# Performance work log

Hardware: AMD Instinct MI355X
Metric: run time of the kernel (lower is better)

## Reference

```python
import jax, jax.numpy as jnp
import numpy as np

B, DT, DV, DA = 32768, 768, 512, 384
P, HID, HEADS = 128, 256, 4
HD = P // HEADS
EPS = 1e-5


def _proj_block(x, W, b, lnw, lnb):
    # Linear -> LayerNorm -> ReLU (Dropout is identity in eval)
    h = x @ W.T + b
    mu = jnp.mean(h, axis=-1, keepdims=True)
    var = jnp.var(h, axis=-1, keepdims=True)
    h = lnw * (h - mu) * jax.lax.rsqrt(var + EPS) + lnb
    return jax.nn.relu(h)


def _mha1(q, kv, Wqkv, bqkv, Wo, bo):
    # torch.nn.MultiheadAttention with seq_len=1 for both query and key/value.
    Wq, Wk, Wv = jnp.split(Wqkv, 3, axis=0)
    bq, bk, bv = jnp.split(bqkv, 3, axis=0)
    qp = (q @ Wq.T + bq).reshape(-1, HEADS, HD)   # [B,H,hd]
    kp = (kv @ Wk.T + bk).reshape(-1, HEADS, HD)
    vp = (kv @ Wv.T + bv).reshape(-1, HEADS, HD)
    scores = jnp.einsum('bhd,bhd->bh', qp, kp) * np.float32(1.0 / np.sqrt(HD))
    attn = jax.nn.softmax(scores[..., None], axis=-1)  # single key -> ones
    ctx = (attn * vp).reshape(-1, P)
    return ctx @ Wo.T + bo


def _forward(xt, xv, xa,
             Wt, bt, lnw_t, lnb_t,
             Wv_, bv_, lnw_v, lnb_v,
             Wa, ba, lnw_a, lnb_a,
             W_qkv, b_qkv, W_o, b_o,
             Wg, bg, Wf1, bf1, Wf2, bf2, Wout, bout):
    t = _proj_block(xt, Wt, bt, lnw_t, lnb_t)   # [B,P]
    v = _proj_block(xv, Wv_, bv_, lnw_v, lnb_v)
    a = _proj_block(xa, Wa, ba, lnw_a, lnb_a)
    # branch order: tv, ta, vt, va, at, av
    Qs = jnp.stack([t, t, v, v, a, a])          # [6,B,P]
    KVs = jnp.stack([v, a, t, a, t, v])
    ctx = jax.vmap(_mha1)(Qs, KVs, W_qkv, b_qkv, W_o, b_o)  # [6,B,P]
    ctx_b = jnp.transpose(ctx, (1, 0, 2))       # [B,6,P]
    feats = ctx_b.reshape(-1, 6 * P)
    g = jax.nn.softmax(feats @ Wg.T + bg, axis=-1)          # [B,6]
    gated = (ctx_b * g[:, :, None]).reshape(-1, 6 * P)
    h = jax.nn.relu(gated @ Wf1.T + bf1)
    h = jax.nn.relu(h @ Wf2.T + bf2)
    return h @ Wout.T + bout                    # [B,2]


def setup_inputs() -> dict:
    key = jax.random.key(0)
    ks = jax.random.split(key, 16)
    f32 = jnp.float32
    def n(k, shape, s=0.02):
        return jax.random.normal(k, shape, f32) * s
    return {
        'xt': jax.random.normal(ks[0], (B, DT), f32),
        'xv': jax.random.normal(ks[1], (B, DV), f32),
        'xa': jax.random.normal(ks[2], (B, DA), f32),
        'Wt': n(ks[3], (P, DT)), 'bt': jnp.zeros(P, f32),
        'lnw_t': jnp.ones(P, f32), 'lnb_t': jnp.zeros(P, f32),
        'Wv_': n(ks[4], (P, DV)), 'bv_': jnp.zeros(P, f32),
        'lnw_v': jnp.ones(P, f32), 'lnb_v': jnp.zeros(P, f32),
        'Wa': n(ks[5], (P, DA)), 'ba': jnp.zeros(P, f32),
        'lnw_a': jnp.ones(P, f32), 'lnb_a': jnp.zeros(P, f32),
        'W_qkv': n(ks[6], (6, 3 * P, P)), 'b_qkv': jnp.zeros((6, 3 * P), f32),
        'W_o': n(ks[7], (6, P, P)), 'b_o': jnp.zeros((6, P), f32),
        'Wg': n(ks[8], (6, 6 * P)), 'bg': jnp.zeros(6, f32),
        'Wf1': n(ks[9], (HID, 6 * P)), 'bf1': jnp.zeros(HID, f32),
        'Wf2': n(ks[10], (HID, HID)), 'bf2': jnp.zeros(HID, f32),
        'Wout': n(ks[11], (2, HID)), 'bout': jnp.zeros(2, f32),
    }


def reference(xt, xv, xa, Wt, bt, lnw_t, lnb_t, Wv_, bv_, lnw_v, lnb_v,
              Wa, ba, lnw_a, lnb_a, W_qkv, b_qkv, W_o, b_o,
              Wg, bg, Wf1, bf1, Wf2, bf2, Wout, bout):
    return _forward(xt, xv, xa, Wt, bt, lnw_t, lnb_t, Wv_, bv_, lnw_v, lnb_v,
                    Wa, ba, lnw_a, lnb_a, W_qkv, b_qkv, W_o, b_o,
                    Wg, bg, Wf1, bf1, Wf2, bf2, Wout, bout)
```

## Files before the change

### kernel.cpp

```cpp
#include <hip/hip_runtime.h>
#include <math.h>

#define DI __device__ __forceinline__

namespace {

constexpr int PB = 32768;

typedef _Float16 half_t;
typedef float f32x4 __attribute__((ext_vector_type(4)));
typedef _Float16 f16x8 __attribute__((ext_vector_type(8)));

#define MFMA16 __builtin_amdgcn_mfma_f32_16x16x32_f16

DI void gl16(const void* g, void* l) {
  __builtin_amdgcn_global_load_lds((const __attribute__((address_space(1))) void*)g,
                                   (__attribute__((address_space(3))) void*)l, 16, 0, 0);
}
DI f16x8 asH(f32x4 v) { return __builtin_bit_cast(f16x8, v); }

DI size_t fragIdx1(int c, int k, int P) {
  return (size_t)((k >> 5)*(P >> 4) + (c >> 4))*512
       + ((k >> 3) & 3)*128 + (c & 15)*8 + (k & 7);
}


__global__ void k_weff(const float* __restrict__ Wqkv, const float* __restrict__ bqkv,
                       const float* __restrict__ Wo, const float* __restrict__ bo,
                       float* __restrict__ M, float* __restrict__ beff)
{
  const int i = blockIdx.x >> 7;
  const int c = blockIdx.x & 127;
  const int k = threadIdx.x;
  const float* wo_row = Wo + (size_t)(i*128 + c)*128;
  const float* wv = Wqkv + (size_t)(i*384 + 256)*128;
  float acc = 0.f;
#pragma unroll 4
  for (int j = 0; j < 128; ++j)
    acc = fmaf(wo_row[j], wv[j*128 + k], acc);
  M[(size_t)(i*128 + c)*128 + k] = acc;

  __shared__ float red[128];
  const float* bv = bqkv + i*384 + 256;
  red[k] = wo_row[k] * bv[k];
  __syncthreads();
  for (int s = 64; s > 0; s >>= 1) {
    if (k < s) red[k] += red[k + s];
    __syncthreads();
  }
  if (k == 0) beff[i*128 + c] = red[0] + bo[i*128 + c];
}

__global__ void k_nbig2(const float* __restrict__ Wf1, const float* __restrict__ M,
                        const float* __restrict__ beff, half_t* __restrict__ Nf)
{
  const int i = blockIdx.x >> 8;
  const int c = blockIdx.x & 255;
  const int k = threadIdx.x;
  const float* w_row = Wf1 + (size_t)c*768 + i*128;
  const float* Mi = M + (size_t)i*128*128;
  float acc = 0.f;
#pragma unroll 4
  for (int j = 0; j < 128; ++j)
    acc = fmaf(w_row[j], Mi[j*128 + k], acc);
  Nf[fragIdx1(c, i*128 + k, 256)] = (half_t)(acc * 4096.f);

  __shared__ float red[128];
  red[k] = w_row[k] * beff[i*128 + k];
  __syncthreads();
  for (int s = 64; s > 0; s >>= 1) {
    if (k < s) red[k] += red[k + s];
    __syncthreads();
  }
  if (k == 0)
    Nf[fragIdx1(c, 768 + i, 256)] = (half_t)(red[0] * 4096.f);
  if (i == 0 && k < 26)
    Nf[fragIdx1(c, 774 + k, 256)] = (half_t)0.f;
}

__global__ void k_ghat(const float* __restrict__ M, const float* __restrict__ Wg,
                       float* __restrict__ Ghat)
{
  const int j = blockIdx.x / 3;
  const int src = blockIdx.x % 3;
  const int k = threadIdx.x;
  int i0, i1;
  if (src == 0)      { i0 = 2; i1 = 4; }
  else if (src == 1) { i0 = 0; i1 = 5; }
  else               { i0 = 1; i1 = 3; }
  float acc = 0.f;
  for (int t = 0; t < 2; ++t) {
    const int i = t ? i1 : i0;
    const float* Mi = M + (size_t)i*128*128;
    const float* wg = Wg + j*768 + i*128;
#pragma unroll 4
    for (int c = 0; c < 128; ++c)
      acc = fmaf(Mi[c*128 + k], wg[c], acc);
  }
  Ghat[j*384 + src*128 + k] = acc;
}

__global__ void k_svec(const float* __restrict__ beff, const float* __restrict__ Wg,
                       const float* __restrict__ bg, float* __restrict__ svec)
{
  const int j = blockIdx.x;
  const int c = threadIdx.x;
  float p = 0.f;
#pragma unroll
  for (int i = 0; i < 6; ++i)
    p = fmaf(beff[i*128 + c], Wg[j*768 + i*128 + c], p);
  __shared__ float red[128];
  red[c] = p;
  __syncthreads();
  for (int s = 64; s > 0; s >>= 1) {
    if (c < s) red[c] += red[c + s];
    __syncthreads();
  }
  if (c == 0) svec[j] = red[0] + bg[j];
}

__global__ void k_splitf(const float* __restrict__ in, half_t* __restrict__ outb,
                         float scale, int P, int KD)
{
  const int idx = blockIdx.x*256 + threadIdx.x;
  if (idx >= P*KD) return;
  const int c = idx / KD, k = idx - c*KD;
  outb[fragIdx1(c, k, P)] = (half_t)(in[idx] * scale);
}

template<int KD>
DI void proj_body(const float* __restrict__ X, const half_t* __restrict__ BF,
                  const float* __restrict__ bias,
                  const float* __restrict__ lnw, const float* __restrict__ lnb,
                  const float* __restrict__ Ghat, float* __restrict__ tva,
                  float* __restrict__ zpart, int row0, int colOff, int srcIdx,
                  f32x4* Bs)
{
  const int tid = threadIdx.x;
  const int lane = tid & 63, wid = tid >> 6;
  const int l15 = lane & 15, l4 = lane >> 4;
  constexpr int NT = KD >> 5;
  constexpr int NP = NT >> 2;
  const int r0 = row0 + wid*32;

  const float* xr0 = X + (size_t)(r0 + l15)*KD + l4*8;
  const float* xr1 = X + (size_t)(r0 + 16 + l15)*KD + l4*8;

  auto STAGE = [&](int p, int buf) {
    const half_t* s = BF + (size_t)p*16384;
#pragma unroll
    for (int i = 0; i < 4; ++i)
      gl16(s + (size_t)(i*512 + tid)*8, (char*)Bs + buf*32768 + i*8192 + tid*16);
  };

  f32x4 a0[4], a1[4];
  auto LA = [&](int t, f32x4 (&a)[4]) {
    const int tc = (t < NT) ? t : NT - 1;
    const f32x4* p0 = reinterpret_cast<const f32x4*>(xr0 + tc*32);
    const f32x4* p1 = reinterpret_cast<const f32x4*>(xr1 + tc*32);
    a[0] = p0[0]; a[1] = p0[1]; a[2] = p1[0]; a[3] = p1[1];
  };
  auto SPLIT = [&](f32x4 (&a)[4], f16x8& h0, f16x8& l0, f16x8& h1, f16x8& l1) {
#pragma unroll
    for (int j = 0; j < 4; ++j) {
      half_t x;
      x = (half_t)a[0][j]; h0[j]   = x; l0[j]   = (half_t)(a[0][j] - (float)x);
      x = (half_t)a[1][j]; h0[j+4] = x; l0[j+4] = (half_t)(a[1][j] - (float)x);
      x = (half_t)a[2][j]; h1[j]   = x; l1[j]   = (half_t)(a[2][j] - (float)x);
      x = (half_t)a[3][j]; h1[j+4] = x; l1[j+4] = (half_t)(a[3][j] - (float)x);
    }
  };

  f32x4 acc[2][8];
#pragma unroll
  for (int rg = 0; rg < 2; ++rg)
#pragma unroll
    for (int fn = 0; fn < 8; ++fn) acc[rg][fn] = f32x4{0.f, 0.f, 0.f, 0.f};

  STAGE(0, 0);
  LA(0, a0); LA(1, a1);

  for (int p = 0; p < NP; ++p) {
    const int buf = p & 1;
    __syncthreads();
    if (p + 1 < NP) STAGE(p + 1, buf ^ 1);
#pragma unroll
    for (int tl = 0; tl < 4; ++tl) {
      const int t = p*4 + tl;
      f16x8 h0, l0, h1, l1;
      if (tl & 1) { SPLIT(a1, h0, l0, h1, l1); LA(t + 2, a1); }
      else        { SPLIT(a0, h0, l0, h1, l1); LA(t + 2, a0); }
#pragma unroll
      for (int fn = 0; fn < 8; ++fn) {
        f16x8 b = asH(Bs[buf*2048 + (tl*8 + fn)*64 + lane]);
        acc[0][fn] = MFMA16(h0, b, acc[0][fn], 0, 0, 0);
        acc[0][fn] = MFMA16(l0, b, acc[0][fn], 0, 0, 0);
        acc[1][fn] = MFMA16(h1, b, acc[1][fn], 0, 0, 0);
        acc[1][fn] = MFMA16(l1, b, acc[1][fn], 0, 0, 0);
      }
    }
  }

  float bc[8], lw[8], lb[8], gh[6][8];
#pragma unroll
  for (int fn = 0; fn < 8; ++fn) {
    const int c = fn*16 + l15;
    bc[fn] = bias[c]; lw[fn] = lnw[c]; lb[fn] = lnb[c];
#pragma unroll
    for (int j = 0; j < 6; ++j) gh[j][fn] = Ghat[j*384 + colOff + c];
  }
#pragma unroll
  for (int rg = 0; rg < 2; ++rg) {
#pragma unroll
    for (int r = 0; r < 4; ++r) {
      float h[8];
      float s = 0.f, q2 = 0.f;
#pragma unroll
      for (int fn = 0; fn < 8; ++fn) {
        h[fn] = acc[rg][fn][r]*(1.f/256.f) + bc[fn];
        s += h[fn]; q2 = fmaf(h[fn], h[fn], q2);
      }
#pragma unroll
      for (int m = 1; m <= 8; m <<= 1) { s += __shfl_xor(s, m); q2 += __shfl_xor(q2, m); }
      const float mean = s*(1.f/128.f);
      const float var  = q2*(1.f/128.f) - mean*mean;
      const float rstd = rsqrtf(var + 1e-5f);
      float o[8];
#pragma unroll
      for (int fn = 0; fn < 8; ++fn)
        o[fn] = fmaxf(fmaf((h[fn] - mean)*rstd, lw[fn], lb[fn]), 0.f);
      const int grow = r0 + rg*16 + l4*4 + r;
      float* tp = tva + (size_t)grow*384 + colOff;
#pragma unroll
      for (int fn = 0; fn < 8; ++fn) tp[fn*16 + l15] = o[fn];
      float s6[6];
#pragma unroll
      for (int j = 0; j < 6; ++j) {
        float z = 0.f;
#pragma unroll
        for (int fn = 0; fn < 8; ++fn) z = fmaf(o[fn], gh[j][fn], z);
#pragma unroll
        for (int m = 1; m <= 8; m <<= 1) z += __shfl_xor(z, m);
        s6[j] = z;
      }
#pragma unroll
      for (int j = 0; j < 6; ++j)
        if (l15 == j) zpart[(size_t)(srcIdx*PB + grow)*6 + j] = s6[j];
    }
  }
}

__global__ __launch_bounds__(512, 2)
void k_proj(const float* __restrict__ xt, const float* __restrict__ xv,
            const float* __restrict__ xa, const half_t* __restrict__ Wft,
            const half_t* __restrict__ Wfv, const half_t* __restrict__ Wfa,
            const float* __restrict__ bt, const float* __restrict__ lnwt, const float* __restrict__ lnbt,
            const float* __restrict__ bvp, const float* __restrict__ lnwv, const float* __restrict__ lnbv,
            const float* __restrict__ bap, const float* __restrict__ lnwa, const float* __restrict__ lnba,
            const float* __restrict__ Ghat, float* __restrict__ tva, float* __restrict__ zpart)
{
  __shared__ f32x4 Bs[4096];
  const int src = blockIdx.y;
  const int row0 = blockIdx.x * 256;
  if (src == 0)
    proj_body<768>(xt, Wft, bt, lnwt, lnbt, Ghat, tva, zpart, row0, 0, 0, Bs);
  else if (src == 1)
    proj_body<512>(xv, Wfv, bvp, lnwv, lnbv, Ghat, tva, zpart, row0, 128, 1, Bs);
  else
    proj_body<384>(xa, Wfa, bap, lnwa, lnba, Ghat, tva, zpart, row0, 256, 2, Bs);
}

__global__ void k_gate2(const float* __restrict__ zp, const float* __restrict__ svec,
                        float* __restrict__ g)
{
  const int r = blockIdx.x*256 + threadIdx.x;
  float z[6];
#pragma unroll
  for (int j = 0; j < 6; ++j)
    z[j] = zp[(size_t)r*6 + j] + zp[(size_t)(PB + r)*6 + j] + zp[(size_t)(2*PB + r)*6 + j] + svec[j];
  float mx = z[0];
#pragma unroll
  for (int j = 1; j < 6; ++j) mx = fmaxf(mx, z[j]);
  float e[6], s = 0.f;
#pragma unroll
  for (int j = 0; j < 6; ++j) { e[j] = expf(z[j] - mx); s += e[j]; }
  const float inv = 1.f / s;
#pragma unroll
  for (int j = 0; j < 6; ++j) g[(size_t)r*6 + j] = e[j]*inv;
}

__global__ __launch_bounds__(256, 3)
void k_f1(const float* __restrict__ tva, const half_t* __restrict__ Nf,
          const float* __restrict__ gbuf, const float* __restrict__ bias,
          half_t* __restrict__ h1h)
{
  __shared__ f32x4 Bs[2048];
  const int tid = threadIdx.x;
  const int row0 = blockIdx.x * 128;
  const int colOff = blockIdx.y * 128;
  const int fn0 = colOff >> 4;
  const int lane = tid & 63, wid = tid >> 6;
  const int l15 = lane & 15, l4 = lane >> 4;
  const int r0 = row0 + wid*32;

  const float* ar0 = tva + (size_t)(r0 + l15)*384 + l4*8;
  const float* ar1 = tva + (size_t)(r0 + 16 + l15)*384 + l4*8;

  f32x4 a0[4], a1[4];
  auto LA = [&](int t, f32x4 (&a)[4]) {
    const int tc = (t < 24) ? t : 23;
    const int koff = ((0x102021 >> ((tc >> 2)*4)) & 3)*128 + (tc & 3)*32;
    const f32x4* p0 = reinterpret_cast<const f32x4*>(ar0 + koff);
    const f32x4* p1 = reinterpret_cast<const f32x4*>(ar1 + koff);
    a[0] = p0[0]; a[1] = p0[1]; a[2] = p1[0]; a[3] = p1[1];
  };
  auto SPLITG = [&](f32x4 (&a)[4], float s0, float s1,
                    f16x8& h0, f16x8& l0, f16x8& h1, f16x8& l1) {
#pragma unroll
    for (int j = 0; j < 4; ++j) {
      float v; half_t x;
      v = a[0][j]*s0; x = (half_t)v; h0[j]   = x; l0[j]   = (half_t)(v - (float)x);
      v = a[1][j]*s0; x = (half_t)v; h0[j+4] = x; l0[j+4] = (half_t)(v - (float)x);
      v = a[2][j]*s1; x = (half_t)v; h1[j]   = x; l1[j]   = (half_t)(v - (float)x);
      v = a[3][j]*s1; x = (half_t)v; h1[j+4] = x; l1[j+4] = (half_t)(v - (float)x);
    }
  };

  f32x4 acc[2][8];
#pragma unroll
  for (int rg = 0; rg < 2; ++rg)
#pragma unroll
    for (int fn = 0; fn < 8; ++fn) acc[rg][fn] = f32x4{0.f, 0.f, 0.f, 0.f};

  LA(0, a0); LA(1, a1);

  for (int q = 0; q < 6; ++q) {
    const float sq0 = gbuf[(size_t)(r0 + l15)*6 + q] * 16.f;
    const float sq1 = gbuf[(size_t)(r0 + 16 + l15)*6 + q] * 16.f;
    __syncthreads();
#pragma unroll
    for (int p = 0; p < 4; ++p) {
      const half_t* sp = Nf + ((size_t)(q*4 + p)*16 + fn0)*512;
#pragma unroll
      for (int i = 0; i < 2; ++i)
        gl16(sp + i*2048 + tid*8, (char*)Bs + p*8192 + i*4096 + wid*1024);
    }
    __syncthreads();
#pragma unroll
    for (int p = 0; p < 4; ++p) {
      const int t = q*4 + p;
      f16x8 h0, l0, h1, l1;
      if (p & 1) { SPLITG(a1, sq0, sq1, h0, l0, h1, l1); LA(t + 2, a1); }
      else       { SPLITG(a0, sq0, sq1, h0, l0, h1, l1); LA(t + 2, a0); }
#pragma unroll
      for (int fn = 0; fn < 8; ++fn) {
        f16x8 b = asH(Bs[(p*8 + fn)*64 + lane]);
        acc[0][fn] = MFMA16(h0, b, acc[0][fn], 0, 0, 0);
        acc[0][fn] = MFMA16(l0, b, acc[0][fn], 0, 0, 0);
        acc[1][fn] = MFMA16(h1, b, acc[1][fn], 0, 0, 0);
        acc[1][fn] = MFMA16(l1, b, acc[1][fn], 0, 0, 0);
      }
    }
  }

  __syncthreads();
  {
    const half_t* sT = Nf + ((size_t)24*16 + fn0)*512;
#pragma unroll
    for (int i = 0; i < 2; ++i)
      gl16(sT + i*2048 + tid*8, (char*)Bs + i*4096 + wid*1024);
  }
  __syncthreads();
  {
    f16x8 h0, h1;
#pragma unroll
    for (int j = 0; j < 8; ++j) {
      h0[j] = (l4 == 0 && j < 6) ? (half_t)(gbuf[(size_t)(r0 + l15)*6 + j]*16.f) : (half_t)0.f;
      h1[j] = (l4 == 0 && j < 6) ? (half_t)(gbuf[(size_t)(r0 + 16 + l15)*6 + j]*16.f) : (half_t)0.f;
    }
#pragma unroll
    for (int fn = 0; fn < 8; ++fn) {
      f16x8 b = asH(Bs[fn*64 + lane]);
      acc[0][fn] = MFMA16(h0, b, acc[0][fn], 0, 0, 0);
      acc[1][fn] = MFMA16(h1, b, acc[1][fn], 0, 0, 0);
    }
  }

  float bc[8];
#pragma unroll
  for (int fn = 0; fn < 8; ++fn) bc[fn] = bias[colOff + fn*16 + l15];
#pragma unroll
  for (int rg = 0; rg < 2; ++rg)
#pragma unroll
    for (int fn = 0; fn < 8; ++fn)
#pragma unroll
      for (int r = 0; r < 4; ++r) {
        float v = acc[rg][fn][r]*(1.f/65536.f) + bc[fn];
        v = fmaxf(v, 0.f) * 256.f;
        const int grow = r0 + rg*16 + l4*4 + r;
        h1h[(size_t)grow*256 + colOff + fn*16 + l15] = (half_t)v;
      }
}

__global__ __launch_bounds__(256, 3)
void k_f2(const half_t* __restrict__ h1h, const half_t* __restrict__ WF,
          const float* __restrict__ bias, const float* __restrict__ Wout,
          float* __restrict__ part)
{
  __shared__ f32x4 Bs[2048];
  const int tid = threadIdx.x;
  const int row0 = blockIdx.x * 128;
  const int colOff = blockIdx.y * 128;
  const int fn0 = colOff >> 4;
  const int lane = tid & 63, wid = tid >> 6;
  const int l15 = lane & 15, l4 = lane >> 4;
  const int r0 = row0 + wid*32;

  const half_t* hr0 = h1h + (size_t)(r0 + l15)*256 + l4*8;
  const half_t* hr1 = h1h + (size_t)(r0 + 16 + l15)*256 + l4*8;

  f16x8 a0[2], a1[2];
  auto LA = [&](int t, f16x8 (&a)[2]) {
    const int tc = (t < 8) ? t : 7;
    a[0] = *reinterpret_cast<const f16x8*>(hr0 + tc*32);
    a[1] = *reinterpret_cast<const f16x8*>(hr1 + tc*32);
  };

  f32x4 acc[2][8];
#pragma unroll
  for (int rg = 0; rg < 2; ++rg)
#pragma unroll
    for (int fn = 0; fn < 8; ++fn) acc[rg][fn] = f32x4{0.f, 0.f, 0.f, 0.f};

  LA(0, a0); LA(1, a1);

  for (int q = 0; q < 2; ++q) {
    __syncthreads();
#pragma unroll
    for (int p = 0; p < 4; ++p) {
      const half_t* sp = WF + ((size_t)(q*4 + p)*16 + fn0)*512;
#pragma unroll
      for (int i = 0; i < 2; ++i)
        gl16(sp + i*2048 + tid*8, (char*)Bs + p*8192 + i*4096 + wid*1024);
    }
    __syncthreads();
#pragma unroll
    for (int p = 0; p < 4; ++p) {
      const int t = q*4 + p;
      f16x8 h0, h1;
      if (p & 1) { h0 = a1[0]; h1 = a1[1]; LA(t + 2, a1); }
      else       { h0 = a0[0]; h1 = a0[1]; LA(t + 2, a0); }
#pragma unroll
      for (int fn = 0; fn < 8; ++fn) {
        f16x8 b = asH(Bs[(p*8 + fn)*64 + lane]);
        acc[0][fn] = MFMA16(h0, b, acc[0][fn], 0, 0, 0);
        acc[1][fn] = MFMA16(h1, b, acc[1][fn], 0, 0, 0);
      }
    }
  }

  float bc[8], w0[8], w1[8];
#pragma unroll
  for (int fn = 0; fn < 8; ++fn) {
    const int c = colOff + fn*16 + l15;
    bc[fn] = bias[c]; w0[fn] = Wout[c]; w1[fn] = Wout[256 + c];
  }
#pragma unroll
  for (int rg = 0; rg < 2; ++rg)
#pragma unroll
    for (int r = 0; r < 4; ++r) {
      float s0 = 0.f, s1 = 0.f;
#pragma unroll
      for (int fn = 0; fn < 8; ++fn) {
        float hv = fmaxf(acc[rg][fn][r]*(1.f/65536.f) + bc[fn], 0.f);
        s0 = fmaf(hv, w0[fn], s0);
        s1 = fmaf(hv, w1[fn], s1);
      }
#pragma unroll
      for (int m = 1; m <= 8; m <<= 1) { s0 += __shfl_xor(s0, m); s1 += __shfl_xor(s1, m); }
      if (l15 == rg*4 + r) {
        const int grow = r0 + rg*16 + l4*4 + r;
        float* pp = part + ((size_t)blockIdx.y*PB + grow)*2;
        pp[0] = s0; pp[1] = s1;
      }
    }
}

__global__ void k_comb(const float* __restrict__ part, const float* __restrict__ bout,
                       float* __restrict__ out)
{
  const int id = blockIdx.x*256 + threadIdx.x;
  const int j = id & 1;
  float s = bout[j];
#pragma unroll
  for (int s2 = 0; s2 < 2; ++s2) s += part[(size_t)s2*PB*2 + id];
  out[id] = s;
}

}

extern "C" void kernel_launch(void* const* d_in, const int* in_sizes, int n_in,
                              void* d_out, int out_size, void* d_ws, size_t ws_size,
                              hipStream_t stream)
{
  const float* xt   = (const float*)d_in[0];
  const float* xv   = (const float*)d_in[1];
  const float* xa   = (const float*)d_in[2];
  const float* Wt   = (const float*)d_in[3];
  const float* bt   = (const float*)d_in[4];
  const float* lnwt = (const float*)d_in[5];
  const float* lnbt = (const float*)d_in[6];
  const float* Wv   = (const float*)d_in[7];
  const float* bv   = (const float*)d_in[8];
  const float* lnwv = (const float*)d_in[9];
  const float* lnbv = (const float*)d_in[10];
  const float* Wa   = (const float*)d_in[11];
  const float* ba   = (const float*)d_in[12];
  const float* lnwa = (const float*)d_in[13];
  const float* lnba = (const float*)d_in[14];
  const float* Wqkv = (const float*)d_in[15];
  const float* bqkv = (const float*)d_in[16];
  const float* Wo   = (const float*)d_in[17];
  const float* bo   = (const float*)d_in[18];
  const float* Wg   = (const float*)d_in[19];
  const float* bg   = (const float*)d_in[20];
  const float* Wf1  = (const float*)d_in[21];
  const float* bf1  = (const float*)d_in[22];
  const float* Wf2  = (const float*)d_in[23];
  const float* bf2  = (const float*)d_in[24];
  const float* Woutp= (const float*)d_in[25];
  const float* boutp= (const float*)d_in[26];
  float* out = (float*)d_out;

  float* ws   = (float*)d_ws;
  float* tva  = ws;
  float* g    = tva  + (size_t)PB*384;
  float* h1pf = g    + (size_t)PB*6;
  float* M    = h1pf + (size_t)PB*128;
  float* beff = M    + 98304;
  half_t* Wft = (half_t*)(beff + 768);
  half_t* Wfv = Wft + 98304;
  half_t* Wfa = Wfv + 65536;
  half_t* Nf  = Wfa + 49152;
  half_t* WF2 = Nf + 204800;
  float* Ghat = (float*)(WF2 + 65536);
  float* svec = Ghat + 2304;
  half_t* h1h = (half_t*)h1pf;
  float* zpart = h1pf;
  float* part  = tva;

  k_weff<<<768, 128, 0, stream>>>(Wqkv, bqkv, Wo, bo, M, beff);
  k_nbig2<<<1536, 128, 0, stream>>>(Wf1, M, beff, Nf);
  k_ghat<<<18, 128, 0, stream>>>(M, Wg, Ghat);
  k_svec<<<6, 128, 0, stream>>>(beff, Wg, bg, svec);
  k_splitf<<<(128*768 + 255)/256, 256, 0, stream>>>(Wt, Wft, 256.f, 128, 768);
  k_splitf<<<(128*512 + 255)/256, 256, 0, stream>>>(Wv, Wfv, 256.f, 128, 512);
  k_splitf<<<(128*384 + 255)/256, 256, 0, stream>>>(Wa, Wfa, 256.f, 128, 384);
  k_splitf<<<(256*256 + 255)/256, 256, 0, stream>>>(Wf2, WF2, 256.f, 256, 256);

  k_proj<<<dim3(128, 3), 512, 0, stream>>>(xt, xv, xa, Wft, Wfv, Wfa,
                                           bt, lnwt, lnbt, bv, lnwv, lnbv, ba, lnwa, lnba,
                                           Ghat, tva, zpart);

  k_gate2<<<PB/256, 256, 0, stream>>>(zpart, svec, g);

  k_f1<<<dim3(256, 2), 256, 0, stream>>>(tva, Nf, g, bf1, h1h);
  k_f2<<<dim3(256, 2), 256, 0, stream>>>(h1h, WF2, bf2, Woutp, part);
  k_comb<<<256, 256, 0, stream>>>(part, boutp, out);
}
```

Baseline: 175.0 us.

## Merge small prep kernels, shrink proj blocks, reorder f1/f2 grid

Merges k_ghat and k_svec into one launch and folds the four weight-split launches into one, cutting six launches to two. k_proj goes from 512-thread to 256-thread blocks covering 128 rows, with half-size LDS staging per phase and more blocks per CU. k_f1/k_f2 grids are transposed so the two column blocks of the same rows run next to each other, which should improve L2 reuse of activation rows. Smaller proj blocks mean more weight restaging per row and more barriers per K step.

After: 214.1 us. 1.22x slower.

```diff
diff --git a/kernel.cpp b/kernel.cpp
--- a/kernel.cpp
+++ b/kernel.cpp
@@ -78,54 +78,60 @@
     Nf[fragIdx1(c, 774 + k, 256)] = (half_t)0.f;
 }
 
-__global__ void k_ghat(const float* __restrict__ M, const float* __restrict__ Wg,
-                       float* __restrict__ Ghat)
-{
-  const int j = blockIdx.x / 3;
-  const int src = blockIdx.x % 3;
+__global__ void k_gsv(const float* __restrict__ M, const float* __restrict__ Wg,
+                      const float* __restrict__ beff, const float* __restrict__ bg,
+                      float* __restrict__ Ghat, float* __restrict__ svec)
+{
+  const int bid = blockIdx.x;
   const int k = threadIdx.x;
-  int i0, i1;
-  if (src == 0)      { i0 = 2; i1 = 4; }
-  else if (src == 1) { i0 = 0; i1 = 5; }
-  else               { i0 = 1; i1 = 3; }
-  float acc = 0.f;
-  for (int t = 0; t < 2; ++t) {
-    const int i = t ? i1 : i0;
-    const float* Mi = M + (size_t)i*128*128;
-    const float* wg = Wg + j*768 + i*128;
+  if (bid < 18) {
+    const int j = bid / 3;
+    const int src = bid % 3;
+    int i0, i1;
+    if (src == 0)      { i0 = 2; i1 = 4; }
+    else if (src == 1) { i0 = 0; i1 = 5; }
+    else               { i0 = 1; i1 = 3; }
+    float acc = 0.f;
+    for (int t = 0; t < 2; ++t) {
+      const int i = t ? i1 : i0;
+      const float* Mi = M + (size_t)i*128*128;
+      const float* wg = Wg + j*768 + i*128;
 #pragma unroll 4
-    for (int c = 0; c < 128; ++c)
-      acc = fmaf(Mi[c*128 + k], wg[c], acc);
-  }
-  Ghat[j*384 + src*128 + k] = acc;
-}
-
-__global__ void k_svec(const float* __restrict__ beff, const float* __restrict__ Wg,
-                       const float* __restrict__ bg, float* __restrict__ svec)
-{
-  const int j = blockIdx.x;
-  const int c = threadIdx.x;
-  float p = 0.f;
-#pragma unroll
-  for (int i = 0; i < 6; ++i)
-    p = fmaf(beff[i*128 + c], Wg[j*768 + i*128 + c], p);
-  __shared__ float red[128];
-  red[c] = p;
-  __syncthreads();
-  for (int s = 64; s > 0; s >>= 1) {
-    if (c < s) red[c] += red[c + s];
-    __syncthreads();
-  }
-  if (c == 0) svec[j] = red[0] + bg[j];
-}
-
-__global__ void k_splitf(const float* __restrict__ in, half_t* __restrict__ outb,
-                         float scale, int P, int KD)
+      for (int c = 0; c < 128; ++c)
+        acc = fmaf(Mi[c*128 + k], wg[c], acc);
+    }
+    Ghat[j*384 + src*128 + k] = acc;
+  } else {
+    const int j = bid - 18;
+    float p = 0.f;
+#pragma unroll
+    for (int i = 0; i < 6; ++i)
+      p = fmaf(beff[i*128 + k], Wg[j*768 + i*128 + k], p);
+    __shared__ float red[128];
+    red[k] = p;
+    __syncthreads();
+    for (int s = 64; s > 0; s >>= 1) {
+      if (k < s) red[k] += red[k + s];
+      __syncthreads();
+    }
+    if (k == 0) svec[j] = red[0] + bg[j];
+  }
+}
+
+__global__ void k_splitall(const float* __restrict__ Wt, const float* __restrict__ Wv,
+                           const float* __restrict__ Wa, const float* __restrict__ Wf2,
+                           half_t* __restrict__ Wft, half_t* __restrict__ Wfv,
+                           half_t* __restrict__ Wfa, half_t* __restrict__ WF2)
 {
   const int idx = blockIdx.x*256 + threadIdx.x;
-  if (idx >= P*KD) return;
-  const int c = idx / KD, k = idx - c*KD;
-  outb[fragIdx1(c, k, P)] = (half_t)(in[idx] * scale);
+  const float* in; half_t* outb; int local, P, KD;
+  if (idx < 98304)        { in = Wt;  outb = Wft; local = idx;          P = 128; KD = 768; }
+  else if (idx < 163840)  { in = Wv;  outb = Wfv; local = idx - 98304;  P = 128; KD = 512; }
+  else if (idx < 212992)  { in = Wa;  outb = Wfa; local = idx - 163840; P = 128; KD = 384; }
+  else if (idx < 278528)  { in = Wf2; outb = WF2; local = idx - 212992; P = 256; KD = 256; }
+  else return;
+  const int c = local / KD, k = local - c*KD;
+  outb[fragIdx1(c, k, P)] = (half_t)(in[local] * 256.f);
 }
 
 template<int KD>
@@ -140,17 +146,17 @@
   const int lane = tid & 63, wid = tid >> 6;
   const int l15 = lane & 15, l4 = lane >> 4;
   constexpr int NT = KD >> 5;
-  constexpr int NP = NT >> 2;
+  constexpr int NP = NT >> 1;
   const int r0 = row0 + wid*32;
 
   const float* xr0 = X + (size_t)(r0 + l15)*KD + l4*8;
   const float* xr1 = X + (size_t)(r0 + 16 + l15)*KD + l4*8;
 
   auto STAGE = [&](int p, int buf) {
-    const half_t* s = BF + (size_t)p*16384;
+    const half_t* s = BF + (size_t)p*8192;
 #pragma unroll
     for (int i = 0; i < 4; ++i)
-      gl16(s + (size_t)(i*512 + tid)*8, (char*)Bs + buf*32768 + i*8192 + tid*16);
+      gl16(s + (size_t)(i*256 + tid)*8, (char*)Bs + buf*16384 + i*4096 + wid*1024 + lane*16);
   };
 
   f32x4 a0[4], a1[4];
@@ -185,14 +191,14 @@
     __syncthreads();
     if (p + 1 < NP) STAGE(p + 1, buf ^ 1);
 #pragma unroll
-    for (int tl = 0; tl < 4; ++tl) {
-      const int t = p*4 + tl;
+    for (int tl = 0; tl < 2; ++tl) {
+      const int t = p*2 + tl;
       f16x8 h0, l0, h1, l1;
       if (tl & 1) { SPLIT(a1, h0, l0, h1, l1); LA(t + 2, a1); }
       else        { SPLIT(a0, h0, l0, h1, l1); LA(t + 2, a0); }
 #pragma unroll
       for (int fn = 0; fn < 8; ++fn) {
-        f16x8 b = asH(Bs[buf*2048 + (tl*8 + fn)*64 + lane]);
+        f16x8 b = asH(Bs[buf*1024 + (tl*8 + fn)*64 + lane]);
         acc[0][fn] = MFMA16(h0, b, acc[0][fn], 0, 0, 0);
         acc[0][fn] = MFMA16(l0, b, acc[0][fn], 0, 0, 0);
         acc[1][fn] = MFMA16(h1, b, acc[1][fn], 0, 0, 0);
@@ -250,7 +256,7 @@
   }
 }
 
-__global__ __launch_bounds__(512, 2)
+__global__ __launch_bounds__(256, 4)
 void k_proj(const float* __restrict__ xt, const float* __restrict__ xv,
             const float* __restrict__ xa, const half_t* __restrict__ Wft,
             const half_t* __restrict__ Wfv, const half_t* __restrict__ Wfa,
@@ -259,9 +265,9 @@
             const float* __restrict__ bap, const float* __restrict__ lnwa, const float* __restrict__ lnba,
             const float* __restrict__ Ghat, float* __restrict__ tva, float* __restrict__ zpart)
 {
-  __shared__ f32x4 Bs[4096];
+  __shared__ f32x4 Bs[2048];
   const int src = blockIdx.y;
-  const int row0 = blockIdx.x * 256;
+  const int row0 = blockIdx.x * 128;
   if (src == 0)
     proj_body<768>(xt, Wft, bt, lnwt, lnbt, Ghat, tva, zpart, row0, 0, 0, Bs);
   else if (src == 1)
@@ -296,8 +302,8 @@
 {
   __shared__ f32x4 Bs[2048];
   const int tid = threadIdx.x;
-  const int row0 = blockIdx.x * 128;
-  const int colOff = blockIdx.y * 128;
+  const int row0 = blockIdx.y * 128;
+  const int colOff = blockIdx.x * 128;
   const int fn0 = colOff >> 4;
   const int lane = tid & 63, wid = tid >> 6;
   const int l15 = lane & 15, l4 = lane >> 4;
@@ -409,8 +415,8 @@
 {
   __shared__ f32x4 Bs[2048];
   const int tid = threadIdx.x;
-  const int row0 = blockIdx.x * 128;
-  const int colOff = blockIdx.y * 128;
+  const int row0 = blockIdx.y * 128;
+  const int colOff = blockIdx.x * 128;
   const int fn0 = colOff >> 4;
   const int lane = tid & 63, wid = tid >> 6;
   const int l15 = lane & 15, l4 = lane >> 4;
@@ -480,7 +486,7 @@
       for (int m = 1; m <= 8; m <<= 1) { s0 += __shfl_xor(s0, m); s1 += __shfl_xor(s1, m); }
       if (l15 == rg*4 + r) {
         const int grow = r0 + rg*16 + l4*4 + r;
-        float* pp = part + ((size_t)blockIdx.y*PB + grow)*2;
+        float* pp = part + ((size_t)blockIdx.x*PB + grow)*2;
         pp[0] = s0; pp[1] = s1;
       }
     }
@@ -551,20 +557,16 @@
 
   k_weff<<<768, 128, 0, stream>>>(Wqkv, bqkv, Wo, bo, M, beff);
   k_nbig2<<<1536, 128, 0, stream>>>(Wf1, M, beff, Nf);
-  k_ghat<<<18, 128, 0, stream>>>(M, Wg, Ghat);
-  k_svec<<<6, 128, 0, stream>>>(beff, Wg, bg, svec);
-  k_splitf<<<(128*768 + 255)/256, 256, 0, stream>>>(Wt, Wft, 256.f, 128, 768);
-  k_splitf<<<(128*512 + 255)/256, 256, 0, stream>>>(Wv, Wfv, 256.f, 128, 512);
-  k_splitf<<<(128*384 + 255)/256, 256, 0, stream>>>(Wa, Wfa, 256.f, 128, 384);
-  k_splitf<<<(256*256 + 255)/256, 256, 0, stream>>>(Wf2, WF2, 256.f, 256, 256);
-
-  k_proj<<<dim3(128, 3), 512, 0, stream>>>(xt, xv, xa, Wft, Wfv, Wfa,
+  k_gsv<<<24, 128, 0, stream>>>(M, Wg, beff, bg, Ghat, svec);
+  k_splitall<<<1088, 256, 0, stream>>>(Wt, Wv, Wa, Wf2, Wft, Wfv, Wfa, WF2);
+
+  k_proj<<<dim3(256, 3), 256, 0, stream>>>(xt, xv, xa, Wft, Wfv, Wfa,
                                            bt, lnwt, lnbt, bv, lnwv, lnbv, ba, lnwa, lnba,
                                            Ghat, tva, zpart);
 
   k_gate2<<<PB/256, 256, 0, stream>>>(zpart, svec, g);
 
-  k_f1<<<dim3(256, 2), 256, 0, stream>>>(tva, Nf, g, bf1, h1h);
-  k_f2<<<dim3(256, 2), 256, 0, stream>>>(h1h, WF2, bf2, Woutp, part);
+  k_f1<<<dim3(2, 256), 256, 0, stream>>>(tva, Nf, g, bf1, h1h);
+  k_f2<<<dim3(2, 256), 256, 0, stream>>>(h1h, WF2, bf2, Woutp, part);
   k_comb<<<256, 256, 0, stream>>>(part, boutp, out);
 }
```
